# Optimization experiments

Hardware: AMD Instinct MI355X
Metric: run time of the kernel (lower is better)

The kernel has to match this reference:

```python
import jax, jax.numpy as jnp
import numpy as np
from jax import lax

EPS = 1e-5  # torch BatchNorm default eps

# Binarization with straight-through estimator (hard-tanh gradient window),
# matching BinaryFunc in dizcza/MCMC_BinaryNet.
@jax.custom_vjp
def binarize(x):
    return jnp.sign(x)

def _bin_fwd(x):
    return jnp.sign(x), x

def _bin_bwd(res, g):
    return (g * (jnp.abs(res) <= 1.0).astype(g.dtype),)

binarize.defvjp(_bin_fwd, _bin_bwd)

def bn2d(x, gamma, beta):
    # training-mode BatchNorm2d: batch stats over (N,H,W), biased variance
    m = x.mean(axis=(0, 2, 3), keepdims=True)
    v = x.var(axis=(0, 2, 3), keepdims=True)
    xn = (x - m) * lax.rsqrt(v + EPS)
    return xn * gamma[None, :, None, None] + beta[None, :, None, None]

def bn1d(x, gamma, beta):
    m = x.mean(axis=0, keepdims=True)
    v = x.var(axis=0, keepdims=True)
    return (x - m) * lax.rsqrt(v + EPS) * gamma[None, :] + beta[None, :]

def bconv(x, w):
    # BinaryDecorator(Conv2d): sign(x) conv sign(W), padding=0, no bias
    return lax.conv_general_dilated(binarize(x), binarize(w), (1, 1), 'VALID',
                                    dimension_numbers=('NCHW', 'OIHW', 'NCHW'))

def maxpool2(x):
    return lax.reduce_window(x, -jnp.inf, lax.max, (1, 1, 2, 2), (1, 1, 2, 2), 'VALID')

def prelu(x, a):
    return jnp.where(x >= 0, x, a * x)


def setup_inputs() -> dict:
    key = jax.random.key(0)
    ks = iter(jax.random.split(key, 16))
    conv_channels = [3, 128, 256, 512]
    fc_sizes = [512 * 6 * 6, 1024, 10]
    d = {'x': jax.random.normal(next(ks), (128, 3, 64, 64), jnp.float32)}
    for i, (cin, cout) in enumerate(zip(conv_channels[:-1], conv_channels[1:])):
        d[f'cg{i}'] = jnp.ones((cin,), jnp.float32)          # BN2d gamma
        d[f'cb{i}'] = jnp.zeros((cin,), jnp.float32)         # BN2d beta
        d[f'cw{i}'] = jax.random.normal(next(ks), (cout, cin, 3, 3), jnp.float32) * 0.05
        d[f'cp{i}'] = jnp.full((1,), 0.25, jnp.float32)      # PReLU (num_parameters=1)
    for i, (fin, fout) in enumerate(zip(fc_sizes[:-1], fc_sizes[1:])):
        d[f'fg{i}'] = jnp.ones((fin,), jnp.float32)
        d[f'fb{i}'] = jnp.zeros((fin,), jnp.float32)
        d[f'fw{i}'] = jax.random.normal(next(ks), (fout, fin), jnp.float32) * 0.05
        d[f'fp{i}'] = jnp.full((1,), 0.25, jnp.float32)
    d['scale'] = jnp.full((1,), 1e-3, jnp.float32)           # ScaleLayer init
    return d


def reference(x, cg0, cb0, cw0, cp0, cg1, cb1, cw1, cp1, cg2, cb2, cw2, cp2,
              fg0, fb0, fw0, fp0, fg1, fb1, fw1, fp1, scale):
    for cg, cb, cw, cp in ((cg0, cb0, cw0, cp0), (cg1, cb1, cw1, cp1), (cg2, cb2, cw2, cp2)):
        x = bn2d(x, cg, cb)
        x = bconv(x, cw)
        x = maxpool2(x)
        x = prelu(x, cp)
    x = x.reshape(x.shape[0], -1)  # [B, 512*6*6]
    for fg, fb, fw, fp in ((fg0, fb0, fw0, fp0), (fg1, fb1, fw1, fp1)):
        x = bn1d(x, fg, fb)
        x = binarize(x) @ binarize(fw).T  # BinaryDecorator(Linear), no bias
        x = prelu(x, fp)
    return x * scale
```

## Files before the change

kernel.cpp:

```cpp
#include <hip/hip_runtime.h>
#include <cstdint>
#include <cstddef>

#define BN_EPS 1e-5


__global__ void zero_d(double* p, int n) {
  int i = blockIdx.x * blockDim.x + threadIdx.x;
  if (i < n) p[i] = 0.0;
}

__global__ void reduce_plane(const float* __restrict__ x, double* __restrict__ sums,
                             int C, int HW) {
  int c = blockIdx.x, n = blockIdx.y;
  const float* p = x + ((long)n * C + c) * HW;
  double s = 0.0, s2 = 0.0;
  for (int i = threadIdx.x; i < HW; i += blockDim.x) {
    double v = (double)p[i];
    s += v; s2 += v * v;
  }
  for (int o = 32; o > 0; o >>= 1) {
    s  += __shfl_down(s, o, 64);
    s2 += __shfl_down(s2, o, 64);
  }
  __shared__ double ls[4], ls2[4];
  int lane = threadIdx.x & 63, w = threadIdx.x >> 6;
  if (lane == 0) { ls[w] = s; ls2[w] = s2; }
  __syncthreads();
  if (threadIdx.x == 0) {
    double a = 0, b = 0;
    for (int i = 0; i < 4; i++) { a += ls[i]; b += ls2[i]; }
    atomicAdd(&sums[2 * c], a);
    atomicAdd(&sums[2 * c + 1], b);
  }
}

__global__ void reduce_cl(const float* __restrict__ x, double* __restrict__ sums,
                          int C, long rows) {
  int lane = threadIdx.x & 63, wv = threadIdx.x >> 6;
  int c = blockIdx.x * 64 + lane;
  double s = 0.0, s2 = 0.0;
  for (long r = blockIdx.y * 4 + wv; r < rows; r += (long)gridDim.y * 4) {
    double v = (double)x[r * C + c];
    s += v; s2 += v * v;
  }
  __shared__ double ls[4][64], ls2[4][64];
  ls[wv][lane] = s; ls2[wv][lane] = s2;
  __syncthreads();
  if (threadIdx.x < 64) {
    double a = ls[0][lane] + ls[1][lane] + ls[2][lane] + ls[3][lane];
    double b = ls2[0][lane] + ls2[1][lane] + ls2[2][lane] + ls2[3][lane];
    atomicAdd(&sums[2 * c], a);
    atomicAdd(&sums[2 * c + 1], b);
  }
}

__global__ void reduce_cols2(const float* __restrict__ x, double* __restrict__ sums,
                             int R, int F, int RS) {
  int f = blockIdx.x * blockDim.x + threadIdx.x;
  int r0 = blockIdx.y * RS, r1 = min(r0 + RS, R);
  double s = 0.0, s2 = 0.0;
  for (int r = r0; r < r1; r++) {
    double v = (double)x[(long)r * F + f];
    s += v; s2 += v * v;
  }
  atomicAdd(&sums[2 * f], s);
  atomicAdd(&sums[2 * f + 1], s2);
}

__global__ void finalize_stats(const double* __restrict__ sums, double2* __restrict__ st,
                               int C, double cnt) {
  int c = blockIdx.x * blockDim.x + threadIdx.x;
  if (c >= C) return;
  double m = sums[2 * c] / cnt;
  double v = sums[2 * c + 1] / cnt - m * m;
  st[c] = make_double2(m, 1.0 / sqrt(v + BN_EPS));
}


__global__ void reduce_a1_i8(const int8_t* __restrict__ a1, int* __restrict__ isums) {
  __shared__ int ls[128][4];
  int t = threadIdx.x;
  if (t < 128) { ls[t][0] = 0; ls[t][1] = 0; ls[t][2] = 0; ls[t][3] = 0; }
  __syncthreads();
  int c4 = (t & 31) * 4, slot = t >> 5;
  int P[4] = {0, 0, 0, 0}, N[4] = {0, 0, 0, 0}, Qp[4] = {0, 0, 0, 0}, Qn[4] = {0, 0, 0, 0};
  for (long r = (long)blockIdx.x * 8 + slot; r < 123008; r += (long)gridDim.x * 8) {
    uint32_t u = *(const uint32_t*)(a1 + r * 128 + c4);
#pragma unroll
    for (int k = 0; k < 4; k++) {
      int d = (int)(int8_t)(u >> (8 * k));
      int dp = max(d, 0), dn = min(d, 0);
      P[k] += dp; N[k] += dn;
      Qp[k] += dp * dp; Qn[k] += dn * dn;
    }
  }
#pragma unroll
  for (int k = 0; k < 4; k++) {
    int c = c4 + k;
    atomicAdd(&ls[c][0], P[k]);  atomicAdd(&ls[c][1], N[k]);
    atomicAdd(&ls[c][2], Qp[k]); atomicAdd(&ls[c][3], Qn[k]);
  }
  __syncthreads();
  if (t < 128) {
    atomicAdd(&isums[4 * t + 0], ls[t][0]);
    atomicAdd(&isums[4 * t + 1], ls[t][1]);
    atomicAdd(&isums[4 * t + 2], ls[t][2]);
    atomicAdd(&isums[4 * t + 3], ls[t][3]);
  }
}

__global__ void finalize_i8(const int* __restrict__ isums, const float* __restrict__ ap,
                            double2* __restrict__ st, double cnt) {
  int c = threadIdx.x;
  double a = (double)ap[0];
  double sum = (double)isums[4 * c] + a * (double)isums[4 * c + 1];
  double sq  = (double)isums[4 * c + 2] + a * a * (double)isums[4 * c + 3];
  double m = sum / cnt;
  double v = sq / cnt - m * m;
  st[c] = make_double2(m, 1.0 / sqrt(v + BN_EPS));
}

__global__ void pack_a1_i8(const int8_t* __restrict__ a1, const double2* __restrict__ st,
                           const float* __restrict__ g, const float* __restrict__ b,
                           const float* __restrict__ ap, uint64_t* __restrict__ out) {
  long wid = (long)blockIdx.x * 4 + (threadIdx.x >> 6);
  if (wid >= 246016L) return;
  int lane = threadIdx.x & 63;
  long row = wid >> 1;
  int c = (int)((wid & 1) * 64 + lane);
  float alpha = ap[0];
  int d = (int)a1[row * 128 + c];
  float v = d >= 0 ? (float)d : alpha * (float)d;
  double2 s = st[c];
  float xn = (float)(((double)v - s.x) * s.y) * g[c] + b[c];
  uint64_t m = __ballot(xn > 0.f);
  if (lane == 0) out[wid] = m;
}


__global__ void pack_bits_c1(const float* __restrict__ x, const double2* __restrict__ st,
                             const float* __restrict__ g, const float* __restrict__ b,
                             uint64_t* __restrict__ rows) {
  int wid = blockIdx.x * 4 + (threadIdx.x >> 6);
  int lane = threadIdx.x & 63;
  int n = wid / 192, rem = wid % 192;
  int ci = rem >> 6, y = rem & 63;
  double2 s = st[ci];
  float xv = x[(((long)n * 3 + ci) * 64 + y) * 64 + lane];
  float xn = (float)(((double)xv - s.x) * s.y) * g[ci] + b[ci];
  uint64_t m = __ballot(xn > 0.f);
  if (lane == 0) rows[wid] = m;
}

__global__ void pack_wc1(const float* __restrict__ w, uint32_t* __restrict__ wm) {
  int co = threadIdx.x;
  uint32_t m = 0;
  for (int j = 0; j < 27; j++) m |= (uint32_t)(w[co * 27 + j] > 0.f) << j;
  wm[co] = m;
}

__global__ void pack_cl(const float* __restrict__ acl, const double2* __restrict__ st,
                        const float* __restrict__ g, const float* __restrict__ b,
                        uint64_t* __restrict__ out, int C, long nwords, int lw) {
  long wid = (long)blockIdx.x * 4 + (threadIdx.x >> 6);
  if (wid >= nwords) return;
  int lane = threadIdx.x & 63;
  long row = wid >> lw;
  int w = (int)(wid & ((1 << lw) - 1));
  int c = w * 64 + lane;
  double2 s = st[c];
  float xv = acl[row * C + c];
  float xn = (float)(((double)xv - s.x) * s.y) * g[c] + b[c];
  uint64_t m = __ballot(xn > 0.f);
  if (lane == 0) out[wid] = m;
}

__global__ void pack_wconv(const float* __restrict__ w, uint64_t* __restrict__ out,
                           int CO, int CI, int W) {
  int i = blockIdx.x * blockDim.x + threadIdx.x;
  int total = CO * 9 * W;
  if (i >= total) return;
  int wd = i % W;
  int t = i / W;
  int tap = t % 9, co = t / 9;
  uint64_t bits = 0;
  for (int k = 0; k < 64; k++) {
    int ci = wd * 64 + k;
    bits |= (uint64_t)(w[((long)co * CI + ci) * 9 + tap] > 0.f) << k;
  }
  out[i] = bits;
}

__global__ void pack_nz(const float* __restrict__ x, const double2* __restrict__ st,
                        const float* __restrict__ g, const float* __restrict__ b,
                        uint64_t* __restrict__ out, int R, int F) {
  int Wf = F >> 6;
  long wid = (long)blockIdx.x * 4 + (threadIdx.x >> 6);
  if (wid >= (long)R * Wf) return;
  int lane = threadIdx.x & 63;
  long r = wid / Wf;
  int w = (int)(wid % Wf);
  int f = w * 64 + lane;
  double2 s = st[f];
  double d = (double)x[r * F + f] - s.x;
  float xn = (float)(d * s.y) * g[f] + b[f];
  uint64_t sm = __ballot(xn > 0.f);
  uint64_t nm = __ballot(d != 0.0);
  if (lane == 0) { out[2 * wid] = sm; out[2 * wid + 1] = nm; }
}

__global__ void pack_wfc2(const float* __restrict__ w, uint64_t* __restrict__ out,
                          int O, int F) {
  int Wf = F >> 6;
  long wid = (long)blockIdx.x * 4 + (threadIdx.x >> 6);
  if (wid >= (long)O * Wf) return;
  int lane = threadIdx.x & 63;
  long o = wid / Wf;
  int wd = (int)(wid % Wf);
  uint64_t m = __ballot(w[o * F + wd * 64 + lane] > 0.f);
  if (lane == 0) out[wid] = m;
}


__global__ __launch_bounds__(256) void conv1_pool3(const uint64_t* __restrict__ rows,
                                                   const uint32_t* __restrict__ wm,
                                                   int8_t* __restrict__ out) {
  __shared__ uint64_t rL[192];
  __shared__ uint32_t wL[128];
  __shared__ uint32_t mL[61 * 4];
  int n = blockIdx.y, chunk = blockIdx.x, t = threadIdx.x;
  if (t < 192) rL[t] = rows[n * 192 + t];
  if (t < 128) wL[t] = wm[t];
  __syncthreads();
  if (t < 244) {
    int pl = t >> 2, quad = t & 3;
    int pos = chunk * 61 + pl;
    if (pos < 961) {
      int py = pos / 31, px = pos - py * 31;
      int cy = 2 * py + (quad >> 1), cx = 2 * px + (quad & 1);
      uint32_t m = 0;
#pragma unroll
      for (int ci = 0; ci < 3; ci++)
#pragma unroll
        for (int ky = 0; ky < 3; ky++)
          m |= (uint32_t)((rL[ci * 64 + cy + ky] >> cx) & 7) << (ci * 9 + ky * 3);
      mL[pl * 4 + quad] = m;
    }
  }
  __syncthreads();
  int co = t & 127, slot = t >> 7;
  uint32_t w = wL[co];
  for (int i = slot; i < 61; i += 2) {
    int pos = chunk * 61 + i;
    if (pos >= 961) break;
    int p0 = __popc(mL[4 * i] ^ w);
    int p1 = __popc(mL[4 * i + 1] ^ w);
    int p2 = __popc(mL[4 * i + 2] ^ w);
    int p3 = __popc(mL[4 * i + 3] ^ w);
    int dot = 27 - 2 * min(min(p0, p1), min(p2, p3));
    out[((long)n * 961 + pos) * 128 + co] = (int8_t)dot;
  }
}

template <int W, int IH>
__device__ __forceinline__ void load_half(uint64_t (&h)[4][2 * W],
                                          const uint64_t* __restrict__ sIn,
                                          int py, int cx) {
#pragma unroll
  for (int cy = 0; cy < 4; cy++) {
    const uint64_t* p = &sIn[((2 * py + cy) * IH + cx) * W];
#pragma unroll
    for (int i = 0; i < 2 * W; i++) h[cy][i] = p[i];
  }
}

template <int W>
__device__ __forceinline__ void conv_quad(const uint64_t (&A)[4][2 * W],
                                          const uint64_t (&B)[4][2 * W],
                                          const uint64_t (&wr)[9 * W],
                                          int& a00, int& a01, int& a10, int& a11) {
  a00 = a01 = a10 = a11 = 0;
#pragma unroll
  for (int cy = 0; cy < 4; cy++) {
#pragma unroll
    for (int dy = 0; dy < 2; dy++) {
      int ky = cy - dy;
      if (ky < 0 || ky > 2) continue;
#pragma unroll
      for (int dx = 0; dx < 2; dx++) {
        int acc = 0;
#pragma unroll
        for (int kx = 0; kx < 3; kx++) {
          int col = dx + kx;
#pragma unroll
          for (int wd = 0; wd < W; wd++) {
            uint64_t pv = (col < 2) ? A[cy][col * W + wd] : B[cy][(col - 2) * W + wd];
            acc += __popcll(pv ^ wr[(ky * 3 + kx) * W + wd]);
          }
        }
        if (dy == 0) { if (dx == 0) a00 += acc; else a01 += acc; }
        else         { if (dx == 0) a10 += acc; else a11 += acc; }
      }
    }
  }
}

template <int W, int IH, int PH, int CHUNK, bool CL>
__global__ __launch_bounds__(256, 2) void convp_slide(
    const uint64_t* __restrict__ in, const uint64_t* __restrict__ wt,
    const float* __restrict__ cp, float* __restrict__ out, int CO) {
  __shared__ uint64_t sIn[IH * IH * W];
  int n = blockIdx.y;
  int cg = blockIdx.x / CHUNK, chunk = blockIdx.x % CHUNK;
  int t = threadIdx.x, lane = t & 63, slot = t >> 6;
  const uint64_t* src = in + (long)n * (IH * IH * W);
  for (int i = t; i < IH * IH * W; i += 256) sIn[i] = src[i];
  int co = cg * 64 + lane;
  uint64_t wr[9 * W];
  const uint64_t* wg = wt + (long)co * (9 * W);
#pragma unroll
  for (int i = 0; i < 9 * W; i++) wr[i] = wg[i];
  __syncthreads();
  int py = chunk * 4 + slot;
  if (py >= PH) return;
  float alpha = cp[0];
  const int K = 9 * 64 * W;
  uint64_t hA[4][2 * W], hB[4][2 * W];
  load_half<W, IH>(hA, sIn, py, 0);
#pragma unroll
  for (int px = 0; px < PH; px += 2) {
    load_half<W, IH>(hB, sIn, py, 2 * px + 2);
    {
      int a00, a01, a10, a11;
      conv_quad<W>(hA, hB, wr, a00, a01, a10, a11);
      int dot = K - 2 * min(min(a00, a01), min(a10, a11));
      float f = (float)dot;
      long idx = CL ? (((long)n * PH * PH + py * PH + px) * CO + co)
                    : (((long)n * CO + co) * PH * PH + py * PH + px);
      out[idx] = dot >= 0 ? f : alpha * f;
    }
    if (px + 1 < PH) {
      load_half<W, IH>(hA, sIn, py, 2 * px + 4);
      int a00, a01, a10, a11;
      conv_quad<W>(hB, hA, wr, a00, a01, a10, a11);
      int dot = K - 2 * min(min(a00, a01), min(a10, a11));
      float f = (float)dot;
      long idx = CL ? (((long)n * PH * PH + py * PH + px + 1) * CO + co)
                    : (((long)n * CO + co) * PH * PH + py * PH + px + 1);
      out[idx] = dot >= 0 ? f : alpha * f;
    }
  }
}


__global__ void fc_bin(const uint64_t* __restrict__ xp, const uint64_t* __restrict__ wp,
                       const float* __restrict__ cp, float* __restrict__ out,
                       int O, int Wf) {
  __shared__ uint64_t xs[288], xz[288];
  int r = blockIdx.y;
  for (int i = threadIdx.x; i < Wf; i += blockDim.x) {
    xs[i] = xp[((long)r * Wf + i) * 2];
    xz[i] = xp[((long)r * Wf + i) * 2 + 1];
  }
  __syncthreads();
  int o = blockIdx.x * blockDim.x + threadIdx.x;
  if (o >= O) return;
  int pc = 0, nzc = 0;
  const uint64_t* wr = wp + (long)o * Wf;
  for (int wd = 0; wd < Wf; wd++) {
    uint64_t nz = xz[wd];
    pc  += __popcll((xs[wd] ^ wr[wd]) & nz);
    nzc += __popcll(nz);
  }
  int dot = nzc - 2 * pc;
  float f = (float)dot;
  float alpha = cp[0];
  out[(long)r * O + o] = dot >= 0 ? f : alpha * f;
}

__global__ void fc_bin_scale(const uint64_t* __restrict__ xp, const uint64_t* __restrict__ wp,
                             const float* __restrict__ cp, const float* __restrict__ scale,
                             float* __restrict__ out, int R, int O, int Wf) {
  int i = blockIdx.x * blockDim.x + threadIdx.x;
  if (i >= R * O) return;
  int o = i % O, r = i / O;
  int pc = 0, nzc = 0;
  for (int wd = 0; wd < Wf; wd++) {
    uint64_t nz = xp[((long)r * Wf + wd) * 2 + 1];
    pc  += __popcll((xp[((long)r * Wf + wd) * 2] ^ wp[(long)o * Wf + wd]) & nz);
    nzc += __popcll(nz);
  }
  int dot = nzc - 2 * pc;
  float f = (float)dot;
  float alpha = cp[0];
  f = dot >= 0 ? f : alpha * f;
  out[i] = f * scale[0];
}


extern "C" void kernel_launch(void* const* d_in, const int* in_sizes, int n_in,
                              void* d_out, int out_size, void* d_ws, size_t ws_size,
                              hipStream_t stream) {
  const float* x   = (const float*)d_in[0];
  const float* cg0 = (const float*)d_in[1];
  const float* cb0 = (const float*)d_in[2];
  const float* cw0 = (const float*)d_in[3];
  const float* cp0 = (const float*)d_in[4];
  const float* cg1 = (const float*)d_in[5];
  const float* cb1 = (const float*)d_in[6];
  const float* cw1 = (const float*)d_in[7];
  const float* cp1 = (const float*)d_in[8];
  const float* cg2 = (const float*)d_in[9];
  const float* cb2 = (const float*)d_in[10];
  const float* cw2 = (const float*)d_in[11];
  const float* cp2 = (const float*)d_in[12];
  const float* fg0 = (const float*)d_in[13];
  const float* fb0 = (const float*)d_in[14];
  const float* fw0 = (const float*)d_in[15];
  const float* fp0 = (const float*)d_in[16];
  const float* fg1 = (const float*)d_in[17];
  const float* fb1 = (const float*)d_in[18];
  const float* fw1 = (const float*)d_in[19];
  const float* fp1 = (const float*)d_in[20];
  const float* scl = (const float*)d_in[21];

  char* ws = (char*)d_ws;
  size_t off = 0;
  auto alloc = [&](size_t bytes) {
    size_t r = off;
    off += (bytes + 255) & ~(size_t)255;
    return r;
  };
  const int C0_OFF = 0, C1_OFF = 16, C2_OFF = 160, C3_OFF = 448, C4_OFF = 18944;
  const int NCH = 19968;

  double*   sums  = (double*)(ws + alloc(((size_t)NCH * 2 + 256) * sizeof(double)));
  int*      isums = (int*)(sums + (size_t)NCH * 2);
  double2*  stats = (double2*)(ws + alloc((size_t)NCH * sizeof(double2)));
  uint64_t* rows0 = (uint64_t*)(ws + alloc(128L * 3 * 64 * 8));
  uint32_t* wm1   = (uint32_t*)(ws + alloc(128L * 4));
  int8_t*   a1    = (int8_t*)(ws + alloc(128L * 961 * 128));
  uint64_t* s1p   = (uint64_t*)(ws + alloc(128L * 961 * 2 * 8));
  uint64_t* w1p   = (uint64_t*)(ws + alloc(256L * 9 * 2 * 8));
  float*    a2    = (float*)(ws + alloc(128L * 196 * 256 * 4));
  uint64_t* s2p   = (uint64_t*)(ws + alloc(128L * 196 * 4 * 8));
  uint64_t* w2p   = (uint64_t*)(ws + alloc(512L * 9 * 4 * 8));
  float*    a3    = (float*)(ws + alloc(128L * 512 * 36 * 4));
  uint64_t* s3p   = (uint64_t*)(ws + alloc(128L * 288 * 2 * 8));
  uint64_t* w3p   = (uint64_t*)(ws + alloc(1024L * 288 * 8));
  float*    f1    = (float*)(ws + alloc(128L * 1024 * 4));
  uint64_t* s4p   = (uint64_t*)(ws + alloc(128L * 16 * 2 * 8));
  uint64_t* w4p   = (uint64_t*)(ws + alloc(10L * 16 * 8));

  const int B = 256;

  zero_d<<<dim3(157), B, 0, stream>>>(sums, NCH * 2 + 256);

  reduce_plane<<<dim3(3, 128), B, 0, stream>>>(x, sums + 2 * C0_OFF, 3, 4096);
  finalize_stats<<<1, 64, 0, stream>>>(sums + 2 * C0_OFF, stats + C0_OFF, 3, 524288.0);
  pack_bits_c1<<<dim3(6144), B, 0, stream>>>(x, stats + C0_OFF, cg0, cb0, rows0);
  pack_wc1<<<1, 128, 0, stream>>>(cw0, wm1);
  conv1_pool3<<<dim3(16, 128), B, 0, stream>>>(rows0, wm1, a1);

  reduce_a1_i8<<<dim3(96), B, 0, stream>>>(a1, isums);
  finalize_i8<<<1, 128, 0, stream>>>(isums, cp0, stats + C1_OFF, 123008.0);
  pack_a1_i8<<<dim3(61504), B, 0, stream>>>(a1, stats + C1_OFF, cg1, cb1, cp0, s1p);
  pack_wconv<<<dim3(18), B, 0, stream>>>(cw1, w1p, 256, 128, 2);
  convp_slide<2, 31, 14, 4, true><<<dim3(16, 128), B, 0, stream>>>(s1p, w1p, cp1, a2, 256);

  reduce_cl<<<dim3(4, 128), B, 0, stream>>>(a2, sums + 2 * C2_OFF, 256, 25088L);
  finalize_stats<<<1, 256, 0, stream>>>(sums + 2 * C2_OFF, stats + C2_OFF, 256, 25088.0);
  pack_cl<<<dim3(25088), B, 0, stream>>>(a2, stats + C2_OFF, cg2, cb2, s2p, 256, 100352L, 2);
  pack_wconv<<<dim3(72), B, 0, stream>>>(cw2, w2p, 512, 256, 4);
  convp_slide<4, 14, 6, 2, false><<<dim3(16, 128), B, 0, stream>>>(s2p, w2p, cp2, a3, 512);

  reduce_cols2<<<dim3(72, 8), B, 0, stream>>>(a3, sums + 2 * C3_OFF, 128, 18432, 16);
  finalize_stats<<<dim3(72), B, 0, stream>>>(sums + 2 * C3_OFF, stats + C3_OFF, 18432, 128.0);
  pack_nz<<<dim3(9216), B, 0, stream>>>(a3, stats + C3_OFF, fg0, fb0, s3p, 128, 18432);
  pack_wfc2<<<dim3(73728), B, 0, stream>>>(fw0, w3p, 1024, 18432);
  fc_bin<<<dim3(4, 128), B, 0, stream>>>(s3p, w3p, fp0, f1, 1024, 288);

  reduce_cols2<<<dim3(4, 8), B, 0, stream>>>(f1, sums + 2 * C4_OFF, 128, 1024, 16);
  finalize_stats<<<dim3(4), B, 0, stream>>>(sums + 2 * C4_OFF, stats + C4_OFF, 1024, 128.0);
  pack_nz<<<dim3(512), B, 0, stream>>>(f1, stats + C4_OFF, fg1, fb1, s4p, 128, 1024);
  pack_wfc2<<<dim3(40), B, 0, stream>>>(fw1, w4p, 10, 1024);
  fc_bin_scale<<<dim3(5), B, 0, stream>>>(s4p, w4p, fp1, scl, (float*)d_out, 128, 10, 16);
}
```

Before: 556.9 us.

## Coalesce weight packing, transpose FC weights, add pooled conv kernel, widen reductions

Conv weights are now packed with one block per output channel staged in shared memory and ballot-based bit packing, replacing per-thread strided 64-element loops. FC1 weights are packed transposed so adjacent threads read adjacent words, and the nonzero count is computed once per row via a shared atomic. Conv3 uses a new per-position pooled kernel, occupancy hints rise to 4 blocks per SM, and the int8 reduction grid grows from 96 to 768 blocks. Together these target uncoalesced global reads and low parallelism, at the cost of more register pressure at the higher occupancy bound.

```diff
diff --git a/kernel.cpp b/kernel.cpp
--- a/kernel.cpp
+++ b/kernel.cpp
@@ -176,20 +176,20 @@
   if (lane == 0) out[wid] = m;
 }
 
-__global__ void pack_wconv(const float* __restrict__ w, uint64_t* __restrict__ out,
-                           int CO, int CI, int W) {
-  int i = blockIdx.x * blockDim.x + threadIdx.x;
-  int total = CO * 9 * W;
-  if (i >= total) return;
-  int wd = i % W;
-  int t = i / W;
-  int tap = t % 9, co = t / 9;
-  uint64_t bits = 0;
-  for (int k = 0; k < 64; k++) {
-    int ci = wd * 64 + k;
-    bits |= (uint64_t)(w[((long)co * CI + ci) * 9 + tap] > 0.f) << k;
-  }
-  out[i] = bits;
+__global__ void pack_wconv2(const float* __restrict__ w, uint64_t* __restrict__ out,
+                            int CI, int W) {
+  __shared__ float sw[2304];
+  int co = blockIdx.x;
+  int total = CI * 9;
+  const float* wc = w + (long)co * total;
+  for (int i = threadIdx.x; i < total; i += blockDim.x) sw[i] = wc[i];
+  __syncthreads();
+  int lane = threadIdx.x & 63, wv = threadIdx.x >> 6;
+  for (int word = wv; word < 9 * W; word += 4) {
+    int tap = word / W, wd = word % W;
+    uint64_t m = __ballot(sw[(wd * 64 + lane) * 9 + tap] > 0.f);
+    if (lane == 0) out[(long)co * 9 * W + word] = m;
+  }
 }
 
 __global__ void pack_nz(const float* __restrict__ x, const double2* __restrict__ st,
@@ -210,6 +210,18 @@
   if (lane == 0) { out[2 * wid] = sm; out[2 * wid + 1] = nm; }
 }
 
+__global__ void pack_wfc2T(const float* __restrict__ w, uint64_t* __restrict__ out,
+                           int O, int F) {
+  int Wf = F >> 6;
+  long wid = (long)blockIdx.x * 4 + (threadIdx.x >> 6);
+  if (wid >= (long)O * Wf) return;
+  int lane = threadIdx.x & 63;
+  long o = wid / Wf;
+  int wd = (int)(wid % Wf);
+  uint64_t m = __ballot(w[o * F + wd * 64 + lane] > 0.f);
+  if (lane == 0) out[(long)wd * O + o] = m;
+}
+
 __global__ void pack_wfc2(const float* __restrict__ w, uint64_t* __restrict__ out,
                           int O, int F) {
   int Wf = F >> 6;
@@ -263,6 +275,7 @@
   }
 }
 
+
 template <int W, int IH>
 __device__ __forceinline__ void load_half(uint64_t (&h)[4][2 * W],
                                           const uint64_t* __restrict__ sIn,
@@ -306,8 +319,8 @@
   }
 }
 
-template <int W, int IH, int PH, int CHUNK, bool CL>
-__global__ __launch_bounds__(256, 2) void convp_slide(
+template <int W, int IH, int PH, int CHUNK>
+__global__ __launch_bounds__(256, 4) void convp_slide(
     const uint64_t* __restrict__ in, const uint64_t* __restrict__ wt,
     const float* __restrict__ cp, float* __restrict__ out, int CO) {
   __shared__ uint64_t sIn[IH * IH * W];
@@ -336,9 +349,7 @@
       conv_quad<W>(hA, hB, wr, a00, a01, a10, a11);
       int dot = K - 2 * min(min(a00, a01), min(a10, a11));
       float f = (float)dot;
-      long idx = CL ? (((long)n * PH * PH + py * PH + px) * CO + co)
-                    : (((long)n * CO + co) * PH * PH + py * PH + px);
-      out[idx] = dot >= 0 ? f : alpha * f;
+      out[((long)n * PH * PH + py * PH + px) * CO + co] = dot >= 0 ? f : alpha * f;
     }
     if (px + 1 < PH) {
       load_half<W, IH>(hA, sIn, py, 2 * px + 4);
@@ -346,34 +357,89 @@
       conv_quad<W>(hB, hA, wr, a00, a01, a10, a11);
       int dot = K - 2 * min(min(a00, a01), min(a10, a11));
       float f = (float)dot;
-      long idx = CL ? (((long)n * PH * PH + py * PH + px + 1) * CO + co)
-                    : (((long)n * CO + co) * PH * PH + py * PH + px + 1);
-      out[idx] = dot >= 0 ? f : alpha * f;
+      out[((long)n * PH * PH + py * PH + px + 1) * CO + co] = dot >= 0 ? f : alpha * f;
     }
   }
 }
 
-
-__global__ void fc_bin(const uint64_t* __restrict__ xp, const uint64_t* __restrict__ wp,
-                       const float* __restrict__ cp, float* __restrict__ out,
-                       int O, int Wf) {
+template <int W, int IH, int PH, int POSCH, bool CL>
+__global__ __launch_bounds__(256, 4) void convp_pool3(
+    const uint64_t* __restrict__ in, const uint64_t* __restrict__ wt,
+    const float* __restrict__ cp, float* __restrict__ out, int CO) {
+  __shared__ uint64_t sIn[IH * IH * W];
+  int n = blockIdx.y;
+  int cg = blockIdx.x / POSCH;
+  int chunk = blockIdx.x % POSCH;
+  int t = threadIdx.x;
+  const uint64_t* src = in + (long)n * (IH * IH * W);
+  for (int i = t; i < IH * IH * W; i += 256) sIn[i] = src[i];
+  int lane = t & 63;
+  int slot = t >> 6;
+  int co = cg * 64 + lane;
+  uint64_t wr[9 * W];
+  const uint64_t* wg = wt + (long)co * (9 * W);
+#pragma unroll
+  for (int i = 0; i < 9 * W; i++) wr[i] = wg[i];
+  __syncthreads();
+  float alpha = cp[0];
+  for (int pos = chunk * 4 + slot; pos < PH * PH; pos += POSCH * 4) {
+    int py = pos / PH, px = pos % PH;
+    int a00 = 0, a01 = 0, a10 = 0, a11 = 0;
+#pragma unroll
+    for (int cy = 0; cy < 4; cy++) {
+      uint64_t row[4 * W];
+      const uint64_t* rp = &sIn[((2 * py + cy) * IH + 2 * px) * W];
+#pragma unroll
+      for (int i = 0; i < 4 * W; i++) row[i] = rp[i];
+#pragma unroll
+      for (int dy = 0; dy < 2; dy++) {
+        int ky = cy - dy;
+        if (ky < 0 || ky > 2) continue;
+#pragma unroll
+        for (int dx = 0; dx < 2; dx++) {
+          int a = 0;
+#pragma unroll
+          for (int kx = 0; kx < 3; kx++)
+#pragma unroll
+            for (int wd = 0; wd < W; wd++)
+              a += __popcll(row[(dx + kx) * W + wd] ^ wr[(ky * 3 + kx) * W + wd]);
+          if (dy == 0) { if (dx == 0) a00 += a; else a01 += a; }
+          else         { if (dx == 0) a10 += a; else a11 += a; }
+        }
+      }
+    }
+    int pmin = min(min(a00, a01), min(a10, a11));
+    int dot = 9 * 64 * W - 2 * pmin;
+    float f = (float)dot;
+    long idx = CL ? (((long)n * PH * PH + pos) * CO + co)
+                  : (((long)n * CO + co) * PH * PH + pos);
+    out[idx] = dot >= 0 ? f : alpha * f;
+  }
+}
+
+
+__global__ void fc_bin2(const uint64_t* __restrict__ xp, const uint64_t* __restrict__ wpT,
+                        const float* __restrict__ cp, float* __restrict__ out,
+                        int O, int Wf) {
   __shared__ uint64_t xs[288], xz[288];
+  __shared__ int nztot;
   int r = blockIdx.y;
+  if (threadIdx.x == 0) nztot = 0;
+  __syncthreads();
+  int lnz = 0;
   for (int i = threadIdx.x; i < Wf; i += blockDim.x) {
-    xs[i] = xp[((long)r * Wf + i) * 2];
-    xz[i] = xp[((long)r * Wf + i) * 2 + 1];
-  }
+    uint64_t sv = xp[((long)r * Wf + i) * 2];
+    uint64_t zv = xp[((long)r * Wf + i) * 2 + 1];
+    xs[i] = sv; xz[i] = zv;
+    lnz += __popcll(zv);
+  }
+  if (lnz) atomicAdd(&nztot, lnz);
   __syncthreads();
   int o = blockIdx.x * blockDim.x + threadIdx.x;
-  if (o >= O) return;
-  int pc = 0, nzc = 0;
-  const uint64_t* wr = wp + (long)o * Wf;
-  for (int wd = 0; wd < Wf; wd++) {
-    uint64_t nz = xz[wd];
-    pc  += __popcll((xs[wd] ^ wr[wd]) & nz);
-    nzc += __popcll(nz);
-  }
-  int dot = nzc - 2 * pc;
+  int pc = 0;
+  for (int wd = 0; wd < Wf; wd++)
+    pc += __popcll((xs[wd] ^ wpT[(long)wd * O + o]) & xz[wd]);
+  int dot = nztot - 2 * pc;
   float f = (float)dot;
   float alpha = cp[0];
   out[(long)r * O + o] = dot >= 0 ? f : alpha * f;
@@ -448,7 +514,7 @@
   uint64_t* w2p   = (uint64_t*)(ws + alloc(512L * 9 * 4 * 8));
   float*    a3    = (float*)(ws + alloc(128L * 512 * 36 * 4));
   uint64_t* s3p   = (uint64_t*)(ws + alloc(128L * 288 * 2 * 8));
-  uint64_t* w3p   = (uint64_t*)(ws + alloc(1024L * 288 * 8));
+  uint64_t* w3pT  = (uint64_t*)(ws + alloc(1024L * 288 * 8));
   float*    f1    = (float*)(ws + alloc(128L * 1024 * 4));
   uint64_t* s4p   = (uint64_t*)(ws + alloc(128L * 16 * 2 * 8));
   uint64_t* w4p   = (uint64_t*)(ws + alloc(10L * 16 * 8));
@@ -463,23 +529,23 @@
   pack_wc1<<<1, 128, 0, stream>>>(cw0, wm1);
   conv1_pool3<<<dim3(16, 128), B, 0, stream>>>(rows0, wm1, a1);
 
-  reduce_a1_i8<<<dim3(96), B, 0, stream>>>(a1, isums);
+  reduce_a1_i8<<<dim3(768), B, 0, stream>>>(a1, isums);
   finalize_i8<<<1, 128, 0, stream>>>(isums, cp0, stats + C1_OFF, 123008.0);
   pack_a1_i8<<<dim3(61504), B, 0, stream>>>(a1, stats + C1_OFF, cg1, cb1, cp0, s1p);
-  pack_wconv<<<dim3(18), B, 0, stream>>>(cw1, w1p, 256, 128, 2);
-  convp_slide<2, 31, 14, 4, true><<<dim3(16, 128), B, 0, stream>>>(s1p, w1p, cp1, a2, 256);
+  pack_wconv2<<<dim3(256), B, 0, stream>>>(cw1, w1p, 128, 2);
+  convp_slide<2, 31, 14, 4><<<dim3(16, 128), B, 0, stream>>>(s1p, w1p, cp1, a2, 256);
 
   reduce_cl<<<dim3(4, 128), B, 0, stream>>>(a2, sums + 2 * C2_OFF, 256, 25088L);
   finalize_stats<<<1, 256, 0, stream>>>(sums + 2 * C2_OFF, stats + C2_OFF, 256, 25088.0);
   pack_cl<<<dim3(25088), B, 0, stream>>>(a2, stats + C2_OFF, cg2, cb2, s2p, 256, 100352L, 2);
-  pack_wconv<<<dim3(72), B, 0, stream>>>(cw2, w2p, 512, 256, 4);
-  convp_slide<4, 14, 6, 2, false><<<dim3(16, 128), B, 0, stream>>>(s2p, w2p, cp2, a3, 512);
+  pack_wconv2<<<dim3(512), B, 0, stream>>>(cw2, w2p, 256, 4);
+  convp_pool3<4, 14, 6, 2, false><<<dim3(16, 128), B, 0, stream>>>(s2p, w2p, cp2, a3, 512);
 
   reduce_cols2<<<dim3(72, 8), B, 0, stream>>>(a3, sums + 2 * C3_OFF, 128, 18432, 16);
   finalize_stats<<<dim3(72), B, 0, stream>>>(sums + 2 * C3_OFF, stats + C3_OFF, 18432, 128.0);
   pack_nz<<<dim3(9216), B, 0, stream>>>(a3, stats + C3_OFF, fg0, fb0, s3p, 128, 18432);
-  pack_wfc2<<<dim3(73728), B, 0, stream>>>(fw0, w3p, 1024, 18432);
-  fc_bin<<<dim3(4, 128), B, 0, stream>>>(s3p, w3p, fp0, f1, 1024, 288);
+  pack_wfc2T<<<dim3(73728), B, 0, stream>>>(fw0, w3pT, 1024, 18432);
+  fc_bin2<<<dim3(4, 128), B, 0, stream>>>(s3p, w3pT, fp0, f1, 1024, 288);
 
   reduce_cols2<<<dim3(4, 8), B, 0, stream>>>(f1, sums + 2 * C4_OFF, 128, 1024, 16);
   finalize_stats<<<dim3(4), B, 0, stream>>>(sums + 2 * C4_OFF, stats + C4_OFF, 1024, 128.0);
```

Result: faster. 543.5 us (-2.4%).
